# Optimization experiments

Measured on AMD Instinct MI355X. Metric: run time of the kernel, lower is better.

Reference implementation:

```python
import jax, jax.numpy as jnp
import numpy as np

D_MODEL = 512
NHEAD = 8
HEAD_DIM = D_MODEL // NHEAD
D_FF = 2048
EPS = 1e-5


def _linear_params(key, d_in, d_out):
    kw, kb = jax.random.split(key)
    bound = 1.0 / np.sqrt(d_in)
    W = jax.random.uniform(kw, (d_out, d_in), jnp.float32, -bound, bound)
    b = jax.random.uniform(kb, (d_out,), jnp.float32, -bound, bound)
    return W, b


def setup_inputs() -> dict:
    key = jax.random.key(0)
    ks = jax.random.split(key, 8)
    src = jax.random.normal(ks[0], (4, 2048, D_MODEL), jnp.float32)
    Wq, bq = _linear_params(ks[1], D_MODEL, D_MODEL)
    Wk, bk = _linear_params(ks[2], D_MODEL, D_MODEL)
    Wv, bv = _linear_params(ks[3], D_MODEL, D_MODEL)
    Wo, bo = _linear_params(ks[4], D_MODEL, D_MODEL)
    W1, b1 = _linear_params(ks[5], D_MODEL, D_FF)
    W2, b2 = _linear_params(ks[6], D_FF, D_MODEL)
    g1 = jnp.ones((D_MODEL,), jnp.float32)
    be1 = jnp.zeros((D_MODEL,), jnp.float32)
    g2 = jnp.ones((D_MODEL,), jnp.float32)
    be2 = jnp.zeros((D_MODEL,), jnp.float32)
    return dict(src=src, Wq=Wq, bq=bq, Wk=Wk, bk=bk, Wv=Wv, bv=bv,
                Wo=Wo, bo=bo, W1=W1, b1=b1, W2=W2, b2=b2,
                g1=g1, be1=be1, g2=g2, be2=be2)


def _layer_norm(x, g, b):
    mu = jnp.mean(x, axis=-1, keepdims=True)
    var = jnp.mean(jnp.square(x - mu), axis=-1, keepdims=True)
    return (x - mu) / jnp.sqrt(var + EPS) * g + b


def reference(src, Wq, bq, Wk, bk, Wv, bv, Wo, bo, W1, b1, W2, b2, g1, be1, g2, be2):
    B, T, D = src.shape
    scale = np.sqrt(HEAD_DIM).astype(np.float32)
    # Projections (torch Linear: x @ W.T + b)
    Q = (src @ Wq.T + bq).reshape(B, T, NHEAD, HEAD_DIM).transpose(0, 2, 1, 3)
    K = (src @ Wk.T + bk).reshape(B, T, NHEAD, HEAD_DIM).transpose(0, 2, 1, 3)
    V = (src @ Wv.T + bv).reshape(B, T, NHEAD, HEAD_DIM).transpose(0, 2, 1, 3)
    # Explicit QK^T -> softmax -> V (no mask, dropout=0)
    scores = jnp.einsum('bhqd,bhkd->bhqk', Q, K) / scale  # (B,H,T,T)
    attn = jax.nn.softmax(scores, axis=-1)
    ctx = jnp.einsum('bhqk,bhkd->bhqd', attn, V)
    ctx = ctx.transpose(0, 2, 1, 3).reshape(B, T, D)
    attn_out = ctx @ Wo.T + bo
    # Add & Norm 1
    x = _layer_norm(src + attn_out, g1, be1)
    # FFN: Linear -> GELU -> Linear
    h = jax.nn.gelu(x @ W1.T + b1, approximate=False)
    ffn_out = h @ W2.T + b2
    # Add & Norm 2
    return _layer_norm(x + ffn_out, g2, be2)
```

## Files before the change

kernel.cpp:

```cpp
#include <hip/hip_runtime.h>
#include <hip/hip_bf16.h>
#include <hip/hip_fp16.h>
#include <math.h>

typedef __bf16 bf16_t;
typedef __bf16 bf16x8 __attribute__((ext_vector_type(8)));
typedef __bf16 bf16x2 __attribute__((ext_vector_type(2)));
typedef float  f32x4  __attribute__((ext_vector_type(4)));

#define D_MODEL 512
#define NHEAD   8
#define HD      64
#define D_FF    2048
#define TOKENS  8192
#define SEQ     2048
#define BATCH   4

__device__ __forceinline__ void gload16(const bf16_t* g, bf16_t* l)
{
    __builtin_amdgcn_global_load_lds(
        (const __attribute__((address_space(1))) void*)g,
        (__attribute__((address_space(3))) void*)l,
        16, 0, 0);
}

__device__ __forceinline__ void cvt4(const float* s, bf16_t* d)
{
    float4 v = *(const float4*)s;
    alignas(8) bf16_t t[4] = {(bf16_t)v.x, (bf16_t)v.y, (bf16_t)v.z, (bf16_t)v.w};
    *(uint2*)d = *(const uint2*)t;
}

__global__ void cvt_weights(const float* __restrict__ src,
                            const float* __restrict__ Wq, const float* __restrict__ Wk,
                            const float* __restrict__ Wv, const float* __restrict__ Wo,
                            const float* __restrict__ W1, const float* __restrict__ W2,
                            const float* __restrict__ bq, const float* __restrict__ bk,
                            const float* __restrict__ bv,
                            bf16_t* __restrict__ Xb,
                            bf16_t* __restrict__ Wqkvb, bf16_t* __restrict__ Wob,
                            bf16_t* __restrict__ W1b, bf16_t* __restrict__ W2b,
                            float* __restrict__ bqkv, float* __restrict__ zbias)
{
    int i = blockIdx.x * 256 + threadIdx.x;
    if (i < 1048576) { cvt4(src + (size_t)i * 4, Xb + (size_t)i * 4); return; }
    i -= 1048576;
    if (i < 65536)        cvt4(Wq + (size_t)i * 4,            Wqkvb + (size_t)i * 4);
    else if (i < 131072)  cvt4(Wk + (size_t)(i - 65536) * 4,  Wqkvb + (size_t)i * 4);
    else if (i < 196608)  cvt4(Wv + (size_t)(i - 131072) * 4, Wqkvb + (size_t)i * 4);
    else if (i < 262144)  cvt4(Wo + (size_t)(i - 196608) * 4, Wob + (size_t)(i - 196608) * 4);
    else if (i < 524288)  cvt4(W1 + (size_t)(i - 262144) * 4, W1b + (size_t)(i - 262144) * 4);
    else if (i < 786432)  cvt4(W2 + (size_t)(i - 524288) * 4, W2b + (size_t)(i - 524288) * 4);
    else if (i < 786816) {
        int j = i - 786432;
        const float* s = (j < 128) ? bq + j * 4 : (j < 256) ? bk + (j - 128) * 4
                                                            : bv + (j - 256) * 4;
        *(float4*)(bqkv + (j & 127) * 4 + (j >> 7) * 512) = *(const float4*)s;
    } else if (i < 786944) {
        int j = i - 786816;
        *(float4*)(zbias + j * 4) = make_float4(0.f, 0.f, 0.f, 0.f);
    }
}

template <int BM, int EPI, bool SPLIT2>
__global__ __launch_bounds__(256)
void gemm_bt(const bf16_t* __restrict__ A, const bf16_t* __restrict__ B,
             const float* __restrict__ bias, const float* __restrict__ biasz,
             void* __restrict__ Cout, int M, int N, int K)
{
    constexpr int MI = BM / 32;
    constexpr int NA = BM / 32;
    __shared__ bf16_t sA[2][BM][64];
    __shared__ bf16_t sB[2][128][64];
    bf16_t* sAf = &sA[0][0][0];
    bf16_t* sBf = &sB[0][0][0];

    const int tid  = threadIdx.x;
    const int wave = tid >> 6;
    const int lane = tid & 63;
    const int g    = lane >> 4;
    const int c16  = lane & 15;
    const int wm   = (wave >> 1) * (BM / 2);
    const int wn   = (wave & 1) * 64;
    const int m0   = blockIdx.y * BM;
    const int n0   = blockIdx.x * 128;

    const int zz    = SPLIT2 ? blockIdx.z : 0;
    const int Keff  = SPLIT2 ? (K >> 1) : K;
    const int kbase = zz * Keff;
    const float* bptr = (SPLIT2 && zz) ? biasz : bias;

    const f32x4 fz = {0.f, 0.f, 0.f, 0.f};
    f32x4 acc[MI][4];
#pragma unroll
    for (int i = 0; i < MI; i++)
#pragma unroll
        for (int j = 0; j < 4; j++) acc[i][j] = fz;

    const bf16_t* gA[NA]; int fa[NA];
#pragma unroll
    for (int i = 0; i < NA; i++) {
        const int f = i * 256 + tid, row = f >> 3, l = (f & 7) ^ (row & 7);
        fa[i] = f;
        gA[i] = A + (size_t)(m0 + row) * K + kbase + l * 8;
    }
    const bf16_t* gB[4]; int fb[4];
#pragma unroll
    for (int i = 0; i < 4; i++) {
        const int f = i * 256 + tid, row = f >> 3, l = (f & 7) ^ (row & 7);
        fb[i] = f;
        gB[i] = B + (size_t)(n0 + row) * K + kbase + l * 8;
    }

#pragma unroll
    for (int i = 0; i < NA; i++) gload16(gA[i], sAf + fa[i] * 8);
#pragma unroll
    for (int i = 0; i < 4; i++)  gload16(gB[i], sBf + fb[i] * 8);

    const int NS = Keff >> 6;
    for (int s = 0; s < NS; ++s) {
        const int cur = s & 1;
        __syncthreads();
        if (s + 1 < NS) {
            const int ko = (s + 1) * 64;
            bf16_t* dA = sAf + (cur ^ 1) * (BM * 64);
            bf16_t* dB = sBf + (cur ^ 1) * 8192;
#pragma unroll
            for (int i = 0; i < NA; i++) gload16(gA[i] + ko, dA + fa[i] * 8);
#pragma unroll
            for (int i = 0; i < 4; i++)  gload16(gB[i] + ko, dB + fb[i] * 8);
        }

#pragma unroll
        for (int sub = 0; sub < 2; ++sub) {
            const int ck = (((sub * 4 + g) ^ (c16 & 7))) * 8;
            bf16x8 af[MI], bfr[4];
#pragma unroll
            for (int i = 0; i < MI; i++)
                af[i] = *(const bf16x8*)&sA[cur][wm + i * 16 + c16][ck];
#pragma unroll
            for (int j = 0; j < 4; j++)
                bfr[j] = *(const bf16x8*)&sB[cur][wn + j * 16 + c16][ck];
#pragma unroll
            for (int mi = 0; mi < MI; mi++)
#pragma unroll
                for (int ni = 0; ni < 4; ni++)
                    acc[mi][ni] = __builtin_amdgcn_mfma_f32_16x16x32_bf16(
                        af[mi], bfr[ni], acc[mi][ni], 0, 0, 0);
        }
    }

    __half* outh = (__half*)Cout + (size_t)zz * M * N;
#pragma unroll
    for (int mi = 0; mi < MI; mi++) {
#pragma unroll
        for (int ni = 0; ni < 4; ni++) {
            const int col = n0 + wn + ni * 16 + c16;
            const float bv = bptr[col];
#pragma unroll
            for (int r = 0; r < 4; r++) {
                const int row = m0 + wm + mi * 16 + g * 4 + r;
                float v = acc[mi][ni][r] + bv;
                if (EPI == 1) v = 0.5f * v * (1.f + erff(v * 0.70710678118654752f));
                if (EPI == 2)
                    outh[(size_t)row * N + col] = (__half)v;
                else
                    ((bf16_t*)Cout)[(size_t)row * N + col] = (bf16_t)v;
            }
        }
    }
}

__global__ __launch_bounds__(256)
void transpose_v(const bf16_t* __restrict__ qkv, bf16_t* __restrict__ vt)
{
    __shared__ bf16_t st[64][72];
    const int t0 = blockIdx.x * 64;
    const int bh = blockIdx.y;
    const int b = bh >> 3, h = bh & 7;
    const int tid = threadIdx.x;

    for (int c = tid; c < 512; c += 256) {
        int r = c >> 3, cj = (c & 7) * 8;
        const bf16_t* src = qkv + ((size_t)(b * SEQ + t0 + r)) * 1536 + 1024 + h * 64 + cj;
        *(int4*)&st[r][cj] = *(const int4*)src;
    }
    __syncthreads();
    for (int c = tid; c < 512; c += 256) {
        int d = c >> 3, pj = (c & 7) * 8;
        alignas(16) bf16_t tmp[8];
#pragma unroll
        for (int j = 0; j < 8; j++) {
            int p = pj + j;
            int t = ((p >> 5) << 5) + (((p >> 2) & 1) << 4) + (((p >> 3) & 3) << 2) + (p & 3);
            tmp[j] = st[t][d];
        }
        *(int4*)(vt + ((size_t)(bh * 64 + d)) * SEQ + t0 + pj) = *(const int4*)tmp;
    }
}

__global__ __launch_bounds__(256)
__attribute__((amdgpu_waves_per_eu(2, 2)))
void flash_attn(const bf16_t* __restrict__ qkv, const bf16_t* __restrict__ vt,
                bf16_t* __restrict__ ctx)
{
    __shared__ bf16_t sK[2][64][64];
    __shared__ bf16_t sVt[2][64][64];

    const int bh = blockIdx.y;
    const int b = bh >> 3, h = bh & 7;
    const int q0 = blockIdx.x * 128;
    const int tid = threadIdx.x;
    const int wave = tid >> 6, lane = tid & 63;
    const int g = lane >> 4, c16 = lane & 15;

    const float qscale = 0.125f * 1.4426950408889634f;
    bf16x8 aq[2][2];
#pragma unroll
    for (int qt = 0; qt < 2; qt++)
#pragma unroll
        for (int ks = 0; ks < 2; ks++) {
            bf16x8 v = *(const bf16x8*)(qkv +
                ((size_t)(b * SEQ + q0 + wave * 32 + qt * 16 + c16)) * 1536 +
                h * 64 + ks * 32 + g * 8);
#pragma unroll
            for (int j = 0; j < 8; j++) v[j] = (bf16_t)((float)v[j] * qscale);
            aq[qt][ks] = v;
        }

    const f32x4 fz = {0.f, 0.f, 0.f, 0.f};
    f32x4 acc_oT[4][2];
#pragma unroll
    for (int dt = 0; dt < 4; dt++)
#pragma unroll
        for (int qt = 0; qt < 2; qt++) acc_oT[dt][qt] = fz;
    float l_acc[2] = {0.f, 0.f};

    const int f0 = tid,        r0 = f0 >> 3, l0 = (f0 & 7) ^ (r0 & 7);
    const int f1 = tid + 256,  r1 = f1 >> 3, l1 = (f1 & 7) ^ (r1 & 7);
    const bf16_t* gK0 = qkv + ((size_t)(b * SEQ + r0)) * 1536 + 512 + h * 64 + l0 * 8;
    const bf16_t* gK1 = qkv + ((size_t)(b * SEQ + r1)) * 1536 + 512 + h * 64 + l1 * 8;
    const bf16_t* gV0 = vt + ((size_t)(bh * 64 + r0)) * SEQ + l0 * 8;
    const bf16_t* gV1 = vt + ((size_t)(bh * 64 + r1)) * SEQ + l1 * 8;
    bf16_t* lK = &sK[0][0][0];
    bf16_t* lV = &sVt[0][0][0];

    gload16(gK0, lK + f0 * 8);
    gload16(gK1, lK + f1 * 8);
    gload16(gV0, lV + f0 * 8);
    gload16(gV1, lV + f1 * 8);

    for (int it = 0; it < 32; ++it) {
        const int cur = it & 1;
        __syncthreads();
        if (it < 31) {
            const size_t kv = (size_t)(it + 1) * 64;
            const int bo = (cur ^ 1) * 4096;
            gload16(gK0 + kv * 1536, lK + bo + f0 * 8);
            gload16(gK1 + kv * 1536, lK + bo + f1 * 8);
            gload16(gV0 + kv,        lV + bo + f0 * 8);
            gload16(gV1 + kv,        lV + bo + f1 * 8);
        }

        f32x4 accs[4][2];
#pragma unroll
        for (int tt = 0; tt < 4; tt++)
#pragma unroll
            for (int qt = 0; qt < 2; qt++) accs[tt][qt] = fz;
#pragma unroll
        for (int ks = 0; ks < 2; ks++) {
            const int pc = ((ks * 4 + g) ^ (c16 & 7)) * 8;
#pragma unroll
            for (int tt = 0; tt < 4; tt++) {
                bf16x8 ak = *(const bf16x8*)&sK[cur][tt * 16 + c16][pc];
                accs[tt][0] = __builtin_amdgcn_mfma_f32_16x16x32_bf16(ak, aq[0][ks], accs[tt][0], 0, 0, 0);
                accs[tt][1] = __builtin_amdgcn_mfma_f32_16x16x32_bf16(ak, aq[1][ks], accs[tt][1], 0, 0, 0);
            }
        }

#pragma unroll
        for (int tt = 0; tt < 4; tt++)
#pragma unroll
            for (int qt = 0; qt < 2; qt++) {
                float s = 0.f;
#pragma unroll
                for (int r = 0; r < 4; r++) {
                    float p = __builtin_amdgcn_exp2f(accs[tt][qt][r]);
                    accs[tt][qt][r] = p;
                    s += p;
                }
                l_acc[qt] += s;
            }
        bf16x8 pb[2][2];
#pragma unroll
        for (int qt = 0; qt < 2; qt++)
#pragma unroll
            for (int kv = 0; kv < 2; kv++)
#pragma unroll
                for (int j = 0; j < 8; j++)
                    pb[qt][kv][j] = (bf16_t)accs[kv * 2 + (j >> 2)][qt][j & 3];

#pragma unroll
        for (int kv = 0; kv < 2; kv++) {
            const int pc = ((kv * 4 + g) ^ (c16 & 7)) * 8;
#pragma unroll
            for (int dt = 0; dt < 4; dt++) {
                bf16x8 av = *(const bf16x8*)&sVt[cur][dt * 16 + c16][pc];
                acc_oT[dt][0] = __builtin_amdgcn_mfma_f32_16x16x32_bf16(av, pb[0][kv], acc_oT[dt][0], 0, 0, 0);
                acc_oT[dt][1] = __builtin_amdgcn_mfma_f32_16x16x32_bf16(av, pb[1][kv], acc_oT[dt][1], 0, 0, 0);
            }
        }
    }

#pragma unroll
    for (int qt = 0; qt < 2; qt++) {
        float l = l_acc[qt];
        l += __shfl_xor(l, 16);
        l += __shfl_xor(l, 32);
        const float inv = 1.0f / l;
        const int token = q0 + wave * 32 + qt * 16 + c16;
        bf16_t* dst = ctx + ((size_t)(b * SEQ + token)) * 512 + h * 64 + g * 4;
#pragma unroll
        for (int dt = 0; dt < 4; dt++) {
            alignas(8) bf16_t o4[4];
#pragma unroll
            for (int r = 0; r < 4; r++) o4[r] = (bf16_t)(acc_oT[dt][qt][r] * inv);
            *(uint2*)(dst + dt * 16) = *(const uint2*)o4;
        }
    }
}

__global__ __launch_bounds__(256)
void add_ln3(const float* __restrict__ a, const __half* __restrict__ b,
             const __half* __restrict__ c,
             const float* __restrict__ gamma, const float* __restrict__ beta,
             float* __restrict__ outf, bf16_t* __restrict__ outb)
{
    const int row  = blockIdx.x * 4 + (threadIdx.x >> 6);
    const int lane = threadIdx.x & 63;
    const size_t base = (size_t)row * 512 + lane * 8;

    int4 braw = *(const int4*)(b + base);
    int4 craw = *(const int4*)(c + base);
    const __half* bh = (const __half*)&braw;
    const __half* ch = (const __half*)&craw;

    float v[8];
#pragma unroll
    for (int hh = 0; hh < 2; hh++) {
        float4 av = *(const float4*)(a + base + hh * 4);
        v[hh * 4 + 0] = av.x + (float)bh[hh * 4 + 0] + (float)ch[hh * 4 + 0];
        v[hh * 4 + 1] = av.y + (float)bh[hh * 4 + 1] + (float)ch[hh * 4 + 1];
        v[hh * 4 + 2] = av.z + (float)bh[hh * 4 + 2] + (float)ch[hh * 4 + 2];
        v[hh * 4 + 3] = av.w + (float)bh[hh * 4 + 3] + (float)ch[hh * 4 + 3];
    }

    float s = 0.f;
#pragma unroll
    for (int i = 0; i < 8; i++) s += v[i];
#pragma unroll
    for (int off = 32; off > 0; off >>= 1) s += __shfl_xor(s, off);
    const float mu = s * (1.f / 512.f);

    float q = 0.f;
#pragma unroll
    for (int i = 0; i < 8; i++) { float d = v[i] - mu; q += d * d; }
#pragma unroll
    for (int off = 32; off > 0; off >>= 1) q += __shfl_xor(q, off);
    const float rstd = rsqrtf(q * (1.f / 512.f) + 1e-5f);

    float4 g0 = *(const float4*)(gamma + lane * 8);
    float4 g1 = *(const float4*)(gamma + lane * 8 + 4);
    float4 e0 = *(const float4*)(beta + lane * 8);
    float4 e1 = *(const float4*)(beta + lane * 8 + 4);
    const float gg[8] = {g0.x, g0.y, g0.z, g0.w, g1.x, g1.y, g1.z, g1.w};
    const float ee[8] = {e0.x, e0.y, e0.z, e0.w, e1.x, e1.y, e1.z, e1.w};

    float o[8];
#pragma unroll
    for (int i = 0; i < 8; i++) o[i] = (v[i] - mu) * rstd * gg[i] + ee[i];

    *(float4*)(outf + base)     = make_float4(o[0], o[1], o[2], o[3]);
    *(float4*)(outf + base + 4) = make_float4(o[4], o[5], o[6], o[7]);
    if (outb) {
        alignas(16) bf16_t ob[8];
#pragma unroll
        for (int i = 0; i < 8; i++) ob[i] = (bf16_t)o[i];
        *(int4*)(outb + base) = *(const int4*)ob;
    }
}

extern "C" void kernel_launch(void* const* d_in, const int* in_sizes, int n_in,
                              void* d_out, int out_size, void* d_ws, size_t ws_size,
                              hipStream_t stream)
{
    const float* src = (const float*)d_in[0];
    const float* Wq  = (const float*)d_in[1];  const float* bq  = (const float*)d_in[2];
    const float* Wk  = (const float*)d_in[3];  const float* bk  = (const float*)d_in[4];
    const float* Wv  = (const float*)d_in[5];  const float* bv  = (const float*)d_in[6];
    const float* Wo  = (const float*)d_in[7];  const float* bo  = (const float*)d_in[8];
    const float* W1  = (const float*)d_in[9];  const float* b1  = (const float*)d_in[10];
    const float* W2  = (const float*)d_in[11]; const float* b2  = (const float*)d_in[12];
    const float* g1  = (const float*)d_in[13]; const float* be1 = (const float*)d_in[14];
    const float* g2  = (const float*)d_in[15]; const float* be2 = (const float*)d_in[16];
    float* out = (float*)d_out;

    char* ws = (char*)d_ws;
    size_t off = 0;
    auto alloc = [&](size_t bytes) -> void* {
        void* p = ws + off;
        off = (off + bytes + 255) & ~(size_t)255;
        return p;
    };

    bf16_t* Xb    = (bf16_t*)alloc((size_t)TOKENS * 512 * 2);
    bf16_t* Wqkvb = (bf16_t*)alloc((size_t)1536 * 512 * 2);
    bf16_t* Wob   = (bf16_t*)alloc((size_t)512 * 512 * 2);
    bf16_t* W1b   = (bf16_t*)alloc((size_t)2048 * 512 * 2);
    bf16_t* W2b   = (bf16_t*)alloc((size_t)512 * 2048 * 2);
    float*  bqkv  = (float*)alloc(1536 * 4);
    float*  zbias = (float*)alloc(512 * 4);
    bf16_t* QKV   = (bf16_t*)alloc((size_t)TOKENS * 1536 * 2);
    bf16_t* Vt    = (bf16_t*)alloc((size_t)32 * 64 * SEQ * 2);
    bf16_t* CTX   = (bf16_t*)alloc((size_t)TOKENS * 512 * 2);
    __half* ATTa  = (__half*)alloc((size_t)TOKENS * 512 * 2);
    __half* ATTb  = (__half*)alloc((size_t)TOKENS * 512 * 2);
    float*  X1    = (float*)alloc((size_t)TOKENS * 512 * 4);
    bf16_t* X1b   = (bf16_t*)alloc((size_t)TOKENS * 512 * 2);

    bf16_t* H    = QKV;
    __half* FFNa = ATTa;
    __half* FFNb = ATTb;

    cvt_weights<<<7170, 256, 0, stream>>>(src, Wq, Wk, Wv, Wo, W1, W2, bq, bk, bv,
                                          Xb, Wqkvb, Wob, W1b, W2b, bqkv, zbias);

    gemm_bt<128, 0, false><<<dim3(12, 64), 256, 0, stream>>>(
        Xb, Wqkvb, bqkv, zbias, QKV, TOKENS, 1536, 512);

    transpose_v<<<dim3(32, 32), 256, 0, stream>>>(QKV, Vt);
    flash_attn<<<dim3(16, 32), 256, 0, stream>>>(QKV, Vt, CTX);

    gemm_bt<64, 2, true><<<dim3(4, 128, 2), 256, 0, stream>>>(
        CTX, Wob, bo, zbias, ATTa, TOKENS, 512, 512);

    add_ln3<<<2048, 256, 0, stream>>>(src, ATTa, ATTb, g1, be1, X1, X1b);

    gemm_bt<128, 1, false><<<dim3(16, 64), 256, 0, stream>>>(
        X1b, W1b, b1, zbias, H, TOKENS, 2048, 512);

    gemm_bt<64, 2, true><<<dim3(4, 128, 2), 256, 0, stream>>>(
        H, W2b, b2, zbias, FFNa, TOKENS, 512, 2048);

    add_ln3<<<2048, 256, 0, stream>>>(X1, FFNa, FFNb, g2, be2, out, nullptr);
}
```

Before: 279.9 us.

## Add 256x256-tile 512-thread GEMM for QKV and FFN1 projections

Introduces a new GEMM kernel with 256x256 output tiles, 8 waves each computing 128x64, double-buffered LDS loads via global_load_lds with XOR swizzle, and workgroup index swizzling. It replaces the 128-row gemm_bt for the QKV projection and the first FFN layer (with GELU epilogue). Larger tiles raise arithmetic intensity and reduce redundant global loads. The trade-off is fewer workgroups (192 and 256) on a 256-CU device, higher register pressure from 128 accumulators per lane, 128KB of LDS per block, and uncoalesced scalar bf16 stores in the epilogue.

New measurement: 279.8 us. Within noise of the previous version (-0.0%).

```diff
diff --git a/kernel.cpp b/kernel.cpp
--- a/kernel.cpp
+++ b/kernel.cpp
@@ -30,6 +30,8 @@
     alignas(8) bf16_t t[4] = {(bf16_t)v.x, (bf16_t)v.y, (bf16_t)v.z, (bf16_t)v.w};
     *(uint2*)d = *(const uint2*)t;
 }
+
+__device__ __forceinline__ void barrier_raw() { asm volatile("s_barrier" ::: "memory"); }
 
 __global__ void cvt_weights(const float* __restrict__ src,
                             const float* __restrict__ Wq, const float* __restrict__ Wk,
@@ -62,6 +64,107 @@
     }
 }
 
+template <int EPI>
+__global__ __launch_bounds__(512, 2)
+void gemm256(const bf16_t* __restrict__ A, const bf16_t* __restrict__ B,
+             const float* __restrict__ bias, bf16_t* __restrict__ C,
+             int M, int N, int K)
+{
+    __shared__ bf16_t sA[2][256][64];
+    __shared__ bf16_t sB[2][256][64];
+    bf16_t* sAf = &sA[0][0][0];
+    bf16_t* sBf = &sB[0][0][0];
+
+    const int tid  = threadIdx.x;
+    const int wave = tid >> 6;
+    const int lane = tid & 63;
+    const int g    = lane >> 4;
+    const int c16  = lane & 15;
+    const int wm   = (wave >> 2) * 128;
+    const int wn   = (wave & 3) * 64;
+
+    const int nwg  = gridDim.x * gridDim.y;
+    const int flat = blockIdx.y * gridDim.x + blockIdx.x;
+    const int swz  = (flat & 7) * (nwg >> 3) + (flat >> 3);
+    const int m0   = (swz / gridDim.x) * 256;
+    const int n0   = (swz % gridDim.x) * 256;
+
+    const f32x4 fz = {0.f, 0.f, 0.f, 0.f};
+    f32x4 acc[8][4];
+#pragma unroll
+    for (int i = 0; i < 8; i++)
+#pragma unroll
+        for (int j = 0; j < 4; j++) acc[i][j] = fz;
+
+    const bf16_t* gA[4]; const bf16_t* gB[4]; int fa[4];
+#pragma unroll
+    for (int i = 0; i < 4; i++) {
+        const int f = i * 512 + tid, row = f >> 3, l = (f & 7) ^ (row & 7);
+        fa[i] = f;
+        gA[i] = A + (size_t)(m0 + row) * K + l * 8;
+        gB[i] = B + (size_t)(n0 + row) * K + l * 8;
+    }
+
+    auto stage = [&](int ko, int buf) {
+        bf16_t* dA = sAf + buf * (256 * 64);
+        bf16_t* dB = sBf + buf * (256 * 64);
+#pragma unroll
+        for (int i = 0; i < 4; i++) gload16(gA[i] + ko, dA + fa[i] * 8);
+#pragma unroll
+        for (int i = 0; i < 4; i++) gload16(gB[i] + ko, dB + fa[i] * 8);
+    };
+
+    stage(0, 0);
+    stage(64, 1);
+
+    const int NS = K >> 6;
+    for (int s = 0; s < NS; ++s) {
+        const int cur = s & 1;
+        if (s + 1 < NS) asm volatile("s_waitcnt vmcnt(8)" ::: "memory");
+        else            asm volatile("s_waitcnt vmcnt(0)" ::: "memory");
+        barrier_raw();
+
+#pragma unroll
+        for (int ks = 0; ks < 2; ++ks) {
+            const int ck = ((ks * 4 + g) ^ (c16 & 7)) * 8;
+            bf16x8 af[8], bfr[4];
+#pragma unroll
+            for (int i = 0; i < 8; i++)
+                af[i] = *(const bf16x8*)&sA[cur][wm + i * 16 + c16][ck];
+#pragma unroll
+            for (int j = 0; j < 4; j++)
+                bfr[j] = *(const bf16x8*)&sB[cur][wn + j * 16 + c16][ck];
+#pragma unroll
+            for (int mi = 0; mi < 8; mi++)
+#pragma unroll
+                for (int ni = 0; ni < 4; ni++)
+                    acc[mi][ni] = __builtin_amdgcn_mfma_f32_16x16x32_bf16(
+                        af[mi], bfr[ni], acc[mi][ni], 0, 0, 0);
+        }
+
+        barrier_raw();
+        if (s + 2 < NS) stage((s + 2) << 6, cur);
+    }
+
+    float bcol[4];
+#pragma unroll
+    for (int ni = 0; ni < 4; ni++) bcol[ni] = bias[n0 + wn + ni * 16 + c16];
+#pragma unroll
+    for (int mi = 0; mi < 8; mi++) {
+#pragma unroll
+        for (int ni = 0; ni < 4; ni++) {
+            const int col = n0 + wn + ni * 16 + c16;
+#pragma unroll
+            for (int r = 0; r < 4; r++) {
+                const int row = m0 + wm + mi * 16 + g * 4 + r;
+                float v = acc[mi][ni][r] + bcol[ni];
+                if (EPI == 1) v = 0.5f * v * (1.f + erff(v * 0.70710678118654752f));
+                C[(size_t)row * N + col] = (bf16_t)v;
+            }
+        }
+    }
+}
+
 template <int BM, int EPI, bool SPLIT2>
 __global__ __launch_bounds__(256)
 void gemm_bt(const bf16_t* __restrict__ A, const bf16_t* __restrict__ B,
@@ -435,8 +538,8 @@
     cvt_weights<<<7170, 256, 0, stream>>>(src, Wq, Wk, Wv, Wo, W1, W2, bq, bk, bv,
                                           Xb, Wqkvb, Wob, W1b, W2b, bqkv, zbias);
 
-    gemm_bt<128, 0, false><<<dim3(12, 64), 256, 0, stream>>>(
-        Xb, Wqkvb, bqkv, zbias, QKV, TOKENS, 1536, 512);
+    gemm256<0><<<dim3(6, 32), 512, 0, stream>>>(
+        Xb, Wqkvb, bqkv, QKV, TOKENS, 1536, 512);
 
     transpose_v<<<dim3(32, 32), 256, 0, stream>>>(QKV, Vt);
     flash_attn<<<dim3(16, 32), 256, 0, stream>>>(QKV, Vt, CTX);
@@ -446,8 +549,8 @@
 
     add_ln3<<<2048, 256, 0, stream>>>(src, ATTa, ATTb, g1, be1, X1, X1b);
 
-    gemm_bt<128, 1, false><<<dim3(16, 64), 256, 0, stream>>>(
-        X1b, W1b, b1, zbias, H, TOKENS, 2048, 512);
+    gemm256<1><<<dim3(8, 32), 512, 0, stream>>>(
+        X1b, W1b, b1, H, TOKENS, 2048, 512);
 
     gemm_bt<64, 2, true><<<dim3(4, 128, 2), 256, 0, stream>>>(
         H, W2b, b2, zbias, FFNa, TOKENS, 512, 2048);
```

## Use 256x256 GEMM tiles with raw-barrier prefetch and software-pipeline attention

Applied to the files above, without the earlier changes.

All linear layers now go through a 512-thread GEMM with 256x256 tiles. It prefetches two stages ahead using explicit vmcnt waits and raw s_barrier, and uses a swizzled or paired workgroup-to-tile mapping. Flash attention moves to a 4-deep KV ring buffer and skews its loop so the QK^T MFMAs of one tile overlap the PV MFMAs of the previous tile, with s_setprio around the MFMA section. The goal is more reuse per tile and hiding of global-load and softmax latency. The cost is higher LDS and register pressure, and far fewer workgroups (192 or 128) for the GEMMs, which may underfill the 256 CUs.

Measured after the change: 276.1 us. Within noise of the previous version (-1.4%).

```diff
diff --git a/kernel.cpp b/kernel.cpp
--- a/kernel.cpp
+++ b/kernel.cpp
@@ -30,6 +30,8 @@
     alignas(8) bf16_t t[4] = {(bf16_t)v.x, (bf16_t)v.y, (bf16_t)v.z, (bf16_t)v.w};
     *(uint2*)d = *(const uint2*)t;
 }
+
+__device__ __forceinline__ void barrier_raw() { asm volatile("s_barrier" ::: "memory"); }
 
 __global__ void cvt_weights(const float* __restrict__ src,
                             const float* __restrict__ Wq, const float* __restrict__ Wk,
@@ -62,16 +64,14 @@
     }
 }
 
-template <int BM, int EPI, bool SPLIT2>
-__global__ __launch_bounds__(256)
-void gemm_bt(const bf16_t* __restrict__ A, const bf16_t* __restrict__ B,
+template <int EPI, int SPLIT, bool PAIRN>
+__global__ __launch_bounds__(512, 2)
+void gemm256(const bf16_t* __restrict__ A, const bf16_t* __restrict__ B,
              const float* __restrict__ bias, const float* __restrict__ biasz,
              void* __restrict__ Cout, int M, int N, int K)
 {
-    constexpr int MI = BM / 32;
-    constexpr int NA = BM / 32;
-    __shared__ bf16_t sA[2][BM][64];
-    __shared__ bf16_t sB[2][128][64];
+    __shared__ bf16_t sA[2][256][64];
+    __shared__ bf16_t sB[2][256][64];
     bf16_t* sAf = &sA[0][0][0];
     bf16_t* sBf = &sB[0][0][0];
 
@@ -80,87 +80,98 @@
     const int lane = tid & 63;
     const int g    = lane >> 4;
     const int c16  = lane & 15;
-    const int wm   = (wave >> 1) * (BM / 2);
-    const int wn   = (wave & 1) * 64;
-    const int m0   = blockIdx.y * BM;
-    const int n0   = blockIdx.x * 128;
-
-    const int zz    = SPLIT2 ? blockIdx.z : 0;
-    const int Keff  = SPLIT2 ? (K >> 1) : K;
+    const int wm   = (wave >> 2) * 128;
+    const int wn   = (wave & 3) * 64;
+
+    int m0, n0;
+    if constexpr (PAIRN) {
+        const int flat = blockIdx.y * 2 + blockIdx.x;
+        const int m = ((flat >> 4) << 3) + (flat & 7);
+        const int n = (flat >> 3) & 1;
+        m0 = m * 256; n0 = n * 256;
+    } else {
+        const int nwg  = gridDim.x * gridDim.y;
+        const int flat = blockIdx.y * gridDim.x + blockIdx.x;
+        const int swz  = (flat & 7) * (nwg >> 3) + (flat >> 3);
+        m0 = (swz / gridDim.x) * 256;
+        n0 = (swz % gridDim.x) * 256;
+    }
+
+    const int zz    = (SPLIT > 1) ? blockIdx.z : 0;
+    const int Keff  = K / SPLIT;
     const int kbase = zz * Keff;
-    const float* bptr = (SPLIT2 && zz) ? biasz : bias;
+    const float* bptr = (SPLIT > 1 && zz) ? biasz : bias;
 
     const f32x4 fz = {0.f, 0.f, 0.f, 0.f};
-    f32x4 acc[MI][4];
-#pragma unroll
-    for (int i = 0; i < MI; i++)
+    f32x4 acc[8][4];
+#pragma unroll
+    for (int i = 0; i < 8; i++)
 #pragma unroll
         for (int j = 0; j < 4; j++) acc[i][j] = fz;
 
-    const bf16_t* gA[NA]; int fa[NA];
-#pragma unroll
-    for (int i = 0; i < NA; i++) {
-        const int f = i * 256 + tid, row = f >> 3, l = (f & 7) ^ (row & 7);
+    const bf16_t* gA[4]; const bf16_t* gB[4]; int fa[4];
+#pragma unroll
+    for (int i = 0; i < 4; i++) {
+        const int f = i * 512 + tid, row = f >> 3, l = (f & 7) ^ (row & 7);
         fa[i] = f;
         gA[i] = A + (size_t)(m0 + row) * K + kbase + l * 8;
-    }
-    const bf16_t* gB[4]; int fb[4];
-#pragma unroll
-    for (int i = 0; i < 4; i++) {
-        const int f = i * 256 + tid, row = f >> 3, l = (f & 7) ^ (row & 7);
-        fb[i] = f;
         gB[i] = B + (size_t)(n0 + row) * K + kbase + l * 8;
     }
 
-#pragma unroll
-    for (int i = 0; i < NA; i++) gload16(gA[i], sAf + fa[i] * 8);
-#pragma unroll
-    for (int i = 0; i < 4; i++)  gload16(gB[i], sBf + fb[i] * 8);
+    auto stage = [&](int ko, int buf) {
+        bf16_t* dA = sAf + buf * (256 * 64);
+        bf16_t* dB = sBf + buf * (256 * 64);
+#pragma unroll
+        for (int i = 0; i < 4; i++) gload16(gA[i] + ko, dA + fa[i] * 8);
+#pragma unroll
+        for (int i = 0; i < 4; i++) gload16(gB[i] + ko, dB + fa[i] * 8);
+    };
+
+    stage(0, 0);
+    stage(64, 1);
 
     const int NS = Keff >> 6;
     for (int s = 0; s < NS; ++s) {
         const int cur = s & 1;
-        __syncthreads();
-        if (s + 1 < NS) {
-            const int ko = (s + 1) * 64;
-            bf16_t* dA = sAf + (cur ^ 1) * (BM * 64);
-            bf16_t* dB = sBf + (cur ^ 1) * 8192;
-#pragma unroll
-            for (int i = 0; i < NA; i++) gload16(gA[i] + ko, dA + fa[i] * 8);
-#pragma unroll
-            for (int i = 0; i < 4; i++)  gload16(gB[i] + ko, dB + fb[i] * 8);
-        }
-
-#pragma unroll
-        for (int sub = 0; sub < 2; ++sub) {
-            const int ck = (((sub * 4 + g) ^ (c16 & 7))) * 8;
-            bf16x8 af[MI], bfr[4];
-#pragma unroll
-            for (int i = 0; i < MI; i++)
+        if (s + 1 < NS) asm volatile("s_waitcnt vmcnt(8)" ::: "memory");
+        else            asm volatile("s_waitcnt vmcnt(0)" ::: "memory");
+        barrier_raw();
+
+#pragma unroll
+        for (int ks = 0; ks < 2; ++ks) {
+            const int ck = ((ks * 4 + g) ^ (c16 & 7)) * 8;
+            bf16x8 af[8], bfr[4];
+#pragma unroll
+            for (int i = 0; i < 8; i++)
                 af[i] = *(const bf16x8*)&sA[cur][wm + i * 16 + c16][ck];
 #pragma unroll
             for (int j = 0; j < 4; j++)
                 bfr[j] = *(const bf16x8*)&sB[cur][wn + j * 16 + c16][ck];
 #pragma unroll
-            for (int mi = 0; mi < MI; mi++)
+            for (int mi = 0; mi < 8; mi++)
 #pragma unroll
                 for (int ni = 0; ni < 4; ni++)
                     acc[mi][ni] = __builtin_amdgcn_mfma_f32_16x16x32_bf16(
                         af[mi], bfr[ni], acc[mi][ni], 0, 0, 0);
         }
+
+        barrier_raw();
+        if (s + 2 < NS) stage((s + 2) << 6, cur);
     }
 
     __half* outh = (__half*)Cout + (size_t)zz * M * N;
-#pragma unroll
-    for (int mi = 0; mi < MI; mi++) {
+    float bcol[4];
+#pragma unroll
+    for (int ni = 0; ni < 4; ni++) bcol[ni] = bptr[n0 + wn + ni * 16 + c16];
+#pragma unroll
+    for (int mi = 0; mi < 8; mi++) {
 #pragma unroll
         for (int ni = 0; ni < 4; ni++) {
             const int col = n0 + wn + ni * 16 + c16;
-            const float bv = bptr[col];
 #pragma unroll
             for (int r = 0; r < 4; r++) {
                 const int row = m0 + wm + mi * 16 + g * 4 + r;
-                float v = acc[mi][ni][r] + bv;
+                float v = acc[mi][ni][r] + bcol[ni];
                 if (EPI == 1) v = 0.5f * v * (1.f + erff(v * 0.70710678118654752f));
                 if (EPI == 2)
                     outh[(size_t)row * N + col] = (__half)v;
@@ -204,8 +215,8 @@
 void flash_attn(const bf16_t* __restrict__ qkv, const bf16_t* __restrict__ vt,
                 bf16_t* __restrict__ ctx)
 {
-    __shared__ bf16_t sK[2][64][64];
-    __shared__ bf16_t sVt[2][64][64];
+    __shared__ bf16_t sK[4][64][64];
+    __shared__ bf16_t sVt[4][64][64];
 
     const int bh = blockIdx.y;
     const int b = bh >> 3, h = bh & 7;
@@ -245,24 +256,17 @@
     bf16_t* lK = &sK[0][0][0];
     bf16_t* lV = &sVt[0][0][0];
 
-    gload16(gK0, lK + f0 * 8);
-    gload16(gK1, lK + f1 * 8);
-    gload16(gV0, lV + f0 * 8);
-    gload16(gV1, lV + f1 * 8);
-
-    for (int it = 0; it < 32; ++it) {
-        const int cur = it & 1;
-        __syncthreads();
-        if (it < 31) {
-            const size_t kv = (size_t)(it + 1) * 64;
-            const int bo = (cur ^ 1) * 4096;
-            gload16(gK0 + kv * 1536, lK + bo + f0 * 8);
-            gload16(gK1 + kv * 1536, lK + bo + f1 * 8);
-            gload16(gV0 + kv,        lV + bo + f0 * 8);
-            gload16(gV1 + kv,        lV + bo + f1 * 8);
-        }
-
-        f32x4 accs[4][2];
+    auto stageKV = [&](int t) {
+        const int bo = (t & 3) * 4096;
+        const size_t kv = (size_t)t * 64;
+        gload16(gK0 + kv * 1536, lK + bo + f0 * 8);
+        gload16(gK1 + kv * 1536, lK + bo + f1 * 8);
+        gload16(gV0 + kv,        lV + bo + f0 * 8);
+        gload16(gV1 + kv,        lV + bo + f1 * 8);
+    };
+
+    f32x4 accs[4][2];
+    auto qk_mfma = [&](int cur) {
 #pragma unroll
         for (int tt = 0; tt < 4; tt++)
 #pragma unroll
@@ -277,7 +281,23 @@
                 accs[tt][1] = __builtin_amdgcn_mfma_f32_16x16x32_bf16(ak, aq[1][ks], accs[tt][1], 0, 0, 0);
             }
         }
-
+    };
+
+    bf16x8 pb[2][2];
+    auto pv_mfma = [&](int prv) {
+#pragma unroll
+        for (int kv = 0; kv < 2; kv++) {
+            const int pc = ((kv * 4 + g) ^ (c16 & 7)) * 8;
+#pragma unroll
+            for (int dt = 0; dt < 4; dt++) {
+                bf16x8 av = *(const bf16x8*)&sVt[prv][dt * 16 + c16][pc];
+                acc_oT[dt][0] = __builtin_amdgcn_mfma_f32_16x16x32_bf16(av, pb[0][kv], acc_oT[dt][0], 0, 0, 0);
+                acc_oT[dt][1] = __builtin_amdgcn_mfma_f32_16x16x32_bf16(av, pb[1][kv], acc_oT[dt][1], 0, 0, 0);
+            }
+        }
+    };
+
+    auto softmax_pack = [&]() {
 #pragma unroll
         for (int tt = 0; tt < 4; tt++)
 #pragma unroll
@@ -291,7 +311,6 @@
                 }
                 l_acc[qt] += s;
             }
-        bf16x8 pb[2][2];
 #pragma unroll
         for (int qt = 0; qt < 2; qt++)
 #pragma unroll
@@ -299,18 +318,32 @@
 #pragma unroll
                 for (int j = 0; j < 8; j++)
                     pb[qt][kv][j] = (bf16_t)accs[kv * 2 + (j >> 2)][qt][j & 3];
-
-#pragma unroll
-        for (int kv = 0; kv < 2; kv++) {
-            const int pc = ((kv * 4 + g) ^ (c16 & 7)) * 8;
-#pragma unroll
-            for (int dt = 0; dt < 4; dt++) {
-                bf16x8 av = *(const bf16x8*)&sVt[cur][dt * 16 + c16][pc];
-                acc_oT[dt][0] = __builtin_amdgcn_mfma_f32_16x16x32_bf16(av, pb[0][kv], acc_oT[dt][0], 0, 0, 0);
-                acc_oT[dt][1] = __builtin_amdgcn_mfma_f32_16x16x32_bf16(av, pb[1][kv], acc_oT[dt][1], 0, 0, 0);
-            }
-        }
-    }
+    };
+
+    stageKV(0);
+    stageKV(1);
+    asm volatile("s_waitcnt vmcnt(4)" ::: "memory");
+    barrier_raw();
+    qk_mfma(0);
+    softmax_pack();
+    stageKV(2);
+
+    for (int it = 1; it < 32; ++it) {
+        const int cur = it & 3;
+        const int prv = (it - 1) & 3;
+        if (it < 31) asm volatile("s_waitcnt vmcnt(4)" ::: "memory");
+        else         asm volatile("s_waitcnt vmcnt(0)" ::: "memory");
+        barrier_raw();
+
+        __builtin_amdgcn_s_setprio(1);
+        qk_mfma(cur);
+        pv_mfma(prv);
+        __builtin_amdgcn_s_setprio(0);
+        softmax_pack();
+
+        if (it + 2 < 32) stageKV(it + 2);
+    }
+    pv_mfma(31 & 3);
 
 #pragma unroll
     for (int qt = 0; qt < 2; qt++) {
@@ -435,21 +468,21 @@
     cvt_weights<<<7170, 256, 0, stream>>>(src, Wq, Wk, Wv, Wo, W1, W2, bq, bk, bv,
                                           Xb, Wqkvb, Wob, W1b, W2b, bqkv, zbias);
 
-    gemm_bt<128, 0, false><<<dim3(12, 64), 256, 0, stream>>>(
+    gemm256<0, 1, false><<<dim3(6, 32), 512, 0, stream>>>(
         Xb, Wqkvb, bqkv, zbias, QKV, TOKENS, 1536, 512);
 
     transpose_v<<<dim3(32, 32), 256, 0, stream>>>(QKV, Vt);
     flash_attn<<<dim3(16, 32), 256, 0, stream>>>(QKV, Vt, CTX);
 
-    gemm_bt<64, 2, true><<<dim3(4, 128, 2), 256, 0, stream>>>(
+    gemm256<2, 2, true><<<dim3(2, 32, 2), 512, 0, stream>>>(
         CTX, Wob, bo, zbias, ATTa, TOKENS, 512, 512);
 
     add_ln3<<<2048, 256, 0, stream>>>(src, ATTa, ATTb, g1, be1, X1, X1b);
 
-    gemm_bt<128, 1, false><<<dim3(16, 64), 256, 0, stream>>>(
+    gemm256<1, 1, false><<<dim3(8, 32), 512, 0, stream>>>(
         X1b, W1b, b1, zbias, H, TOKENS, 2048, 512);
 
-    gemm_bt<64, 2, true><<<dim3(4, 128, 2), 256, 0, stream>>>(
+    gemm256<2, 2, true><<<dim3(2, 32, 2), 512, 0, stream>>>(
         H, W2b, b2, zbias, FFNa, TOKENS, 512, 2048);
 
     add_ln3<<<2048, 256, 0, stream>>>(X1, FFNa, FFNb, g2, be2, out, nullptr);
```
